# Kernel optimization log

Measured on AMD Instinct MI355X. Metric: run time of the kernel, lower is better.

## Reference

```python
import jax, jax.numpy as jnp
import numpy as np

HEADS = 4
DIM_HEAD = 32
DIM = 128
HIDDEN = HEADS * DIM_HEAD  # 128
SCALE = DIM_HEAD ** -0.5


def setup_inputs() -> dict:
    key = jax.random.key(0)
    ks = jax.random.split(key, 7)
    b, c, h, w = 4, DIM, 256, 256
    x = jax.random.normal(ks[0], (b, c, h, w), dtype=jnp.float32)
    context = jax.random.normal(ks[1], (b, c, h, w), dtype=jnp.float32)
    # conv1x1 weights stored as [out, in] matrices
    s_in = 1.0 / np.sqrt(DIM)
    Wq = jax.random.uniform(ks[2], (HIDDEN, DIM), jnp.float32, -s_in, s_in)
    Wk = jax.random.uniform(ks[3], (HIDDEN, DIM), jnp.float32, -s_in, s_in)
    Wv = jax.random.uniform(ks[4], (HIDDEN, DIM), jnp.float32, -s_in, s_in)
    s_h = 1.0 / np.sqrt(HIDDEN)
    Wo = jax.random.uniform(ks[5], (DIM, HIDDEN), jnp.float32, -s_h, s_h)
    bo = jax.random.uniform(ks[6], (DIM,), jnp.float32, -s_h, s_h)
    return {"x": x, "context": context, "Wq": Wq, "Wk": Wk, "Wv": Wv, "Wo": Wo, "bo": bo}


def reference(x, context, Wq, Wk, Wv, Wo, bo):
    b, c, h, w = x.shape
    n = h * w
    xf = x.reshape(b, c, n)         # flatten spatial
    cf = context.reshape(b, c, n)
    # conv1x1 projections == channel matmuls
    q = jnp.einsum('oc,bcn->bon', Wq, xf).reshape(b, HEADS, DIM_HEAD, n)
    k = jnp.einsum('oc,bcn->bon', Wk, cf).reshape(b, HEADS, DIM_HEAD, n)
    v = jnp.einsum('oc,bcn->bon', Wv, cf).reshape(b, HEADS, DIM_HEAD, n)
    q = q * SCALE
    k = jax.nn.softmax(k, axis=-1)  # softmax over spatial positions
    ctx = jnp.einsum('bhdn,bhen->bhde', k, v)   # [b,h,d,e] small d_head x d_head
    out = jnp.einsum('bhde,bhdn->bhen', ctx, q)  # [b,h,e,n]
    out = out.reshape(b, HIDDEN, n)
    out = jnp.einsum('oc,bcn->bon', Wo, out) + bo[None, :, None]
    return out.reshape(b, c, h, w)
```

## Files before the change

kernel.cpp:

```cpp
#include <hip/hip_runtime.h>
#include <cstdint>
#include <cstddef>

typedef __bf16 bf16x8 __attribute__((ext_vector_type(8)));
typedef float f32x4 __attribute__((ext_vector_type(4)));
typedef float f32x16 __attribute__((ext_vector_type(16)));
typedef unsigned int u32x2 __attribute__((ext_vector_type(2)));
typedef unsigned int u32x4 __attribute__((ext_vector_type(4)));

#define MFMA16(a, b, c) __builtin_amdgcn_mfma_f32_16x16x32_bf16((a), (b), (c), 0, 0, 0)
#define MFMA32(a, b, c) __builtin_amdgcn_mfma_f32_32x32x16_bf16((a), (b), (c), 0, 0, 0)

#define BAR() asm volatile("s_waitcnt lgkmcnt(0)\n\ts_barrier" ::: "memory")

static constexpr int CD = 128;
static constexpr int NTOK = 65536;
static constexpr float F_SCALE = 0.17677669529663688f;
static constexpr float F_LOG2E = 1.4426950408889634f;
static constexpr int PART = 4224;
static constexpr int NPARTS = 128;

__device__ __forceinline__ unsigned pk2(float a, float b) {
  unsigned short ua = __builtin_bit_cast(unsigned short, (__bf16)a);
  unsigned short ub = __builtin_bit_cast(unsigned short, (__bf16)b);
  return (unsigned)ua | ((unsigned)ub << 16);
}

__device__ __forceinline__ f32x16 z16() {
  f32x16 v;
#pragma unroll
  for (int i = 0; i < 16; ++i) v[i] = 0.f;
  return v;
}

struct Grp { f32x4 M[4]; };

__device__ __forceinline__ Grp load_grp(const float* src, int lane) {
  Grp g;
  const float* p = src + (size_t)((lane >> 4) * 4) * NTOK + (lane & 15) * 4;
#pragma unroll
  for (int v = 0; v < 4; ++v) g.M[v] = *(const f32x4*)(p + (size_t)v * NTOK);
  return g;
}

__device__ __forceinline__ void pack_grp(const Grp& g, char* T2, int cqBase, int lane) {
  int cq = cqBase + (lane >> 4);
  int nq = lane & 15;
#pragma unroll
  for (int j = 0; j < 4; ++j) {
    int n = nq * 4 + j;
    *(u32x2*)(T2 + n * 256 + ((cq * 8) ^ ((((n & 15) ^ (n >> 4))) << 4))) =
        u32x2{pk2(g.M[0][j], g.M[1][j]), pk2(g.M[2][j], g.M[3][j])};
  }
}

struct Grp32 { f32x4 M[4]; };

__device__ __forceinline__ Grp32 load_grp32(const float* src, int lane) {
  Grp32 g;
  int q = (lane >> 3) & 7;
  const float* p = src + (size_t)(2 * q) * NTOK + (lane & 7) * 4;
  g.M[0] = *(const f32x4*)p;
  g.M[1] = *(const f32x4*)(p + NTOK);
  g.M[2] = *(const f32x4*)(p + (size_t)16 * NTOK);
  g.M[3] = *(const f32x4*)(p + (size_t)17 * NTOK);
  return g;
}

__device__ __forceinline__ void pack_grp32(const Grp32& g, char* T2, int cpBase, int lane) {
  int q = (lane >> 3) & 7;
  int a = lane & 7;
#pragma unroll
  for (int j = 0; j < 4; ++j) {
    int n = a * 4 + j;
    int sw = (((n & 15) ^ (n >> 4)) << 4);
    *(unsigned*)(T2 + n * 256 + (((cpBase + q) * 4) ^ sw)) = pk2(g.M[0][j], g.M[1][j]);
    *(unsigned*)(T2 + n * 256 + (((cpBase + 8 + q) * 4) ^ sw)) = pk2(g.M[2][j], g.M[3][j]);
  }
}

__global__ __launch_bounds__(256) __attribute__((amdgpu_waves_per_eu(2)))
void k1_ctx(const float* __restrict__ ctx_in, const float* __restrict__ Wk,
            const float* __restrict__ Wv, float* __restrict__ S_part) {
  __shared__ char smem[32 * 1024];
  const int tid = threadIdx.x;
  const int lane = tid & 63;
  const int w = tid >> 6;
  const int l31 = lane & 31;
  const int l2 = lane >> 5;
  const int b = blockIdx.x >> 7;
  const int cb = blockIdx.x & 127;

  bf16x8 WfK[8], WfV[8];
#pragma unroll
  for (int ks = 0; ks < 8; ++ks) {
    const float* pK = Wk + (size_t)(w * 32 + l31) * CD + ks * 16 + l2 * 8;
    const float* pV = Wv + (size_t)(w * 32 + l31) * CD + ks * 16 + l2 * 8;
#pragma unroll
    for (int e = 0; e < 8; ++e) {
      WfK[ks][e] = (__bf16)(pK[e] * F_LOG2E);
      WfV[ks][e] = (__bf16)pV[e];
    }
  }

  f32x16 Sacc = z16();
  float zacc = 0.f;

  const float* srcA = ctx_in + (size_t)b * CD * NTOK + (size_t)(w * 32) * NTOK + cb * 512;
  const float* srcB = srcA + (size_t)16 * NTOK;

  Grp fa = load_grp(srcA, lane), fb = load_grp(srcB, lane);
#pragma unroll
  for (int s = 0; s < 8; ++s) {
    char* T2 = smem + (s & 1) * 16384;
    pack_grp(fa, T2, w * 8, lane);
    pack_grp(fb, T2, w * 8 + 4, lane);
    if (s < 7) {
      fa = load_grp(srcA + (s + 1) * 64, lane);
      fb = load_grp(srcB + (s + 1) * 64, lane);
    }
    BAR();

    unsigned pe[2][4][2], pv[2][4][2];
#pragma unroll
    for (int t = 0; t < 2; ++t) {
      f32x16 aK = z16(), aV = z16();
#pragma unroll
      for (int ks = 0; ks < 8; ++ks) {
        bf16x8 At = *(const bf16x8*)(
            T2 + (t * 32 + l31) * 256 +
            ((ks * 32 + l2 * 16) ^ (((l31 & 15) ^ (2 * t + (l31 >> 4))) << 4)));
        aK = MFMA32(At, WfK[ks], aK);
        aV = MFMA32(At, WfV[ks], aV);
      }
#pragma unroll
      for (int q = 0; q < 4; ++q) {
        float e0 = __builtin_exp2f(aK[4 * q + 0]);
        float e1 = __builtin_exp2f(aK[4 * q + 1]);
        float e2 = __builtin_exp2f(aK[4 * q + 2]);
        float e3 = __builtin_exp2f(aK[4 * q + 3]);
        zacc += (e0 + e1) + (e2 + e3);
        pe[t][q][0] = pk2(e0, e1);
        pe[t][q][1] = pk2(e2, e3);
        pv[t][q][0] = pk2(aV[4 * q + 0], aV[4 * q + 1]);
        pv[t][q][1] = pk2(aV[4 * q + 2], aV[4 * q + 3]);
      }
    }

#pragma unroll
    for (int nw = 0; nw < 4; ++nw) {
      const int t = nw >> 1, w2 = nw & 1;
      unsigned ea0 = pe[t][2 * w2][0], eb0 = pe[t][2 * w2 + 1][0];
      unsigned ea1 = pe[t][2 * w2][1], eb1 = pe[t][2 * w2 + 1][1];
      asm("v_permlane32_swap_b32 %0, %1" : "+v"(ea0), "+v"(eb0));
      asm("v_permlane32_swap_b32 %0, %1" : "+v"(ea1), "+v"(eb1));
      unsigned va0 = pv[t][2 * w2][0], vb0 = pv[t][2 * w2 + 1][0];
      unsigned va1 = pv[t][2 * w2][1], vb1 = pv[t][2 * w2 + 1][1];
      asm("v_permlane32_swap_b32 %0, %1" : "+v"(va0), "+v"(vb0));
      asm("v_permlane32_swap_b32 %0, %1" : "+v"(va1), "+v"(vb1));
      bf16x8 Ea = __builtin_bit_cast(bf16x8, u32x4{ea0, ea1, eb0, eb1});
      bf16x8 Vb = __builtin_bit_cast(bf16x8, u32x4{va0, va1, vb0, vb1});
      Sacc = MFMA32(Ea, Vb, Sacc);
    }
  }

  float* outp = S_part + (size_t)blockIdx.x * PART;
#pragma unroll
  for (int q = 0; q < 4; ++q) {
    f32x4 v{Sacc[4 * q + 0], Sacc[4 * q + 1], Sacc[4 * q + 2], Sacc[4 * q + 3]};
    *(f32x4*)(outp + w * 1024 + lane * 16 + q * 4) = v;
  }
  zacc += __shfl_xor(zacc, 32, 64);
  if (l2 == 0) outp[4096 + w * 32 + l31] = zacc;
}

__global__ void k2a_reduce(const float* __restrict__ S_part, float* __restrict__ S_red,
                           float* __restrict__ Z_red) {
  int bid = blockIdx.x;
  int b = bid / 33, bs = bid % 33;
  int tid = threadIdx.x;
  __shared__ float red[256];
  int e_loc = tid & 127, half = tid >> 7;
  const float* base =
      S_part + (size_t)b * NPARTS * PART + (bs < 32 ? bs * 128 + e_loc : 4096 + e_loc);
  float sum = 0.f;
  int h = NPARTS >> 1;
  for (int p = half * h; p < half * h + h; ++p) sum += base[(size_t)p * PART];
  red[tid] = sum;
  __syncthreads();
  if (tid < 128) {
    float v = red[tid] + red[tid + 128];
    if (bs < 32)
      S_red[b * 4096 + bs * 128 + tid] = v;
    else
      Z_red[b * 128 + tid] = v;
  }
}

__global__ void k2b_weff(const float* __restrict__ S_red, const float* __restrict__ Z_red,
                         const float* __restrict__ Wq, const float* __restrict__ Wo,
                         float* __restrict__ W_eff) {
  int b = blockIdx.x >> 3, og = blockIdx.x & 7;
  int tid = threadIdx.x;
  __shared__ float ctx_lds[4096];
  __shared__ float T_lds[16 * 128];
  for (int i = tid * 16; i < tid * 16 + 16; ++i) {
    int h = i >> 10, d = (i >> 5) & 31, e = i & 31;
    int fl = h * 1024 + ((e + ((d >> 2) & 1) * 32) << 4) + (d & 3) + ((d >> 3) << 2);
    ctx_lds[i] = S_red[b * 4096 + fl] / Z_red[b * 128 + h * 32 + d];
  }
  __syncthreads();
  {
    int o_loc = tid >> 4, hd0 = (tid & 15) * 8;
    int o = og * 16 + o_loc;
    for (int j = 0; j < 8; ++j) {
      int hd = hd0 + j, h = hd >> 5, d = hd & 31;
      const float* wo = Wo + o * 128 + h * 32;
      const float* cx = ctx_lds + h * 1024 + d * 32;
      float acc = 0.f;
      for (int e = 0; e < 32; ++e) acc += wo[e] * cx[e];
      T_lds[o_loc * 128 + hd] = acc;
    }
  }
  __syncthreads();
  {
    int o_loc = tid >> 4, c0 = (tid & 15) * 8;
    float acc[8] = {};
    const float* Trow = T_lds + o_loc * 128;
    for (int hd = 0; hd < 128; ++hd) {
      float tv = Trow[hd];
      const float* wq = Wq + hd * 128 + c0;
#pragma unroll
      for (int j = 0; j < 8; ++j) acc[j] += tv * wq[j];
    }
    float* op = W_eff + b * 16384 + (og * 16 + o_loc) * 128 + c0;
#pragma unroll
    for (int j = 0; j < 8; ++j) op[j] = F_SCALE * acc[j];
  }
}

__global__ __launch_bounds__(256, 2) void k3_out(const float* __restrict__ x,
                                                 const float* __restrict__ W_eff,
                                                 const float* __restrict__ bo,
                                                 float* __restrict__ out) {
  __shared__ char smem[16 * 1024];
  const int tid = threadIdx.x;
  const int lane = tid & 63;
  const int w = tid >> 6;
  const int l15 = lane & 15;
  const int lg = lane >> 4;
  const int b = blockIdx.x >> 8;
  const int cb = blockIdx.x & 255;

  bf16x8 Wf[2][4];
#pragma unroll
  for (int m = 0; m < 2; ++m) {
    int o = w * 32 + m * 16 + l15;
#pragma unroll
    for (int ks = 0; ks < 4; ++ks) {
      const float* p = W_eff + b * 16384 + o * 128 + ks * 32 + lg * 8;
#pragma unroll
      for (int e = 0; e < 8; ++e) Wf[m][ks][e] = (__bf16)p[e];
    }
  }
  float bof[2] = {bo[w * 32 + l15], bo[w * 32 + 16 + l15]};

  const float* src = x + (size_t)b * CD * NTOK + (size_t)(w * 32) * NTOK + cb * 256;
  float* dst = out + (size_t)b * CD * NTOK + cb * 256;

  Grp32 f0 = load_grp32(src, lane);
  Grp32 f1 = load_grp32(src + 32, lane);
  Grp32 f2 = load_grp32(src + 64, lane);

  f32x4 acc[8][2][2];
#pragma unroll
  for (int s = 0; s < 8; ++s)
#pragma unroll
    for (int t = 0; t < 2; ++t)
#pragma unroll
      for (int m = 0; m < 2; ++m) acc[s][t][m] = f32x4{0.f, 0.f, 0.f, 0.f};

#pragma unroll
  for (int s = 0; s < 8; ++s) {
    char* T2 = smem + (s & 1) * 8192;
    if ((s % 3) == 0) {
      pack_grp32(f0, T2, w * 16, lane);
      if (s + 3 < 8) f0 = load_grp32(src + (s + 3) * 32, lane);
    } else if ((s % 3) == 1) {
      pack_grp32(f1, T2, w * 16, lane);
      if (s + 3 < 8) f1 = load_grp32(src + (s + 3) * 32, lane);
    } else {
      pack_grp32(f2, T2, w * 16, lane);
      if (s + 3 < 8) f2 = load_grp32(src + (s + 3) * 32, lane);
    }
    BAR();

#pragma unroll
    for (int t = 0; t < 2; ++t) {
#pragma unroll
      for (int ks = 0; ks < 4; ++ks) {
        bf16x8 At = *(const bf16x8*)(T2 + (t * 16 + l15) * 256 +
                                     ((ks * 64 + lg * 16) ^ ((l15 ^ t) << 4)));
#pragma unroll
        for (int m = 0; m < 2; ++m) acc[s][t][m] = MFMA16(At, Wf[m][ks], acc[s][t][m]);
      }
    }
  }

#pragma unroll
  for (int m = 0; m < 2; ++m) {
    int o = w * 32 + m * 16 + l15;
    float bb = bof[m];
    float* rowp = dst + (size_t)o * NTOK;
#pragma unroll
    for (int s = 0; s < 8; ++s)
#pragma unroll
      for (int t = 0; t < 2; ++t) {
        f32x4 v = acc[s][t][m];
        v[0] += bb; v[1] += bb; v[2] += bb; v[3] += bb;
        *(f32x4*)(rowp + s * 32 + t * 16 + lg * 4) = v;
      }
  }
}

extern "C" void kernel_launch(void* const* d_in, const int* in_sizes, int n_in,
                              void* d_out, int out_size, void* d_ws, size_t ws_size,
                              hipStream_t stream) {
  const float* x = (const float*)d_in[0];
  const float* ctxg = (const float*)d_in[1];
  const float* Wq = (const float*)d_in[2];
  const float* Wk = (const float*)d_in[3];
  const float* Wv = (const float*)d_in[4];
  const float* Wo = (const float*)d_in[5];
  const float* bo = (const float*)d_in[6];
  float* out = (float*)d_out;

  float* ws = (float*)d_ws;
  float* S_part = ws;
  float* S_red = ws + (size_t)512 * PART;
  float* Z_red = S_red + 16384;
  float* W_eff = Z_red + 512;

  k1_ctx<<<dim3(512), dim3(256), 0, stream>>>(ctxg, Wk, Wv, S_part);
  k2a_reduce<<<dim3(132), dim3(256), 0, stream>>>(S_part, S_red, Z_red);
  k2b_weff<<<dim3(32), dim3(256), 0, stream>>>(S_red, Z_red, Wq, Wo, W_eff);
  k3_out<<<dim3(1024), dim3(256), 0, stream>>>(x, W_eff, bo, out);
}
```

Before: 154.7 us.

## Shrink k1 strips to 32 tokens, halve LDS, raise occupancy and grid size

The context-projection kernel now processes 32-token strips instead of 64, using a 16KB double buffer and the existing 32-row load/pack helpers, with a launch bound targeting 3 blocks per CU. When the workspace is large enough the grid grows to 1024 blocks of 8 strips each, otherwise 512 blocks of 16 strips, and the reduce kernel takes the part count as a parameter. The aim is more resident waves and more blocks to hide global-load latency. The cost is more per-strip barriers, twice as many partial sums to reduce, and a dynamic loop that is no longer unrolled.

```diff
diff --git a/kernel.cpp b/kernel.cpp
--- a/kernel.cpp
+++ b/kernel.cpp
@@ -18,7 +18,6 @@
 static constexpr float F_SCALE = 0.17677669529663688f;
 static constexpr float F_LOG2E = 1.4426950408889634f;
 static constexpr int PART = 4224;
-static constexpr int NPARTS = 128;
 
 __device__ __forceinline__ unsigned pk2(float a, float b) {
   unsigned short ua = __builtin_bit_cast(unsigned short, (__bf16)a);
@@ -31,27 +30,6 @@
 #pragma unroll
   for (int i = 0; i < 16; ++i) v[i] = 0.f;
   return v;
-}
-
-struct Grp { f32x4 M[4]; };
-
-__device__ __forceinline__ Grp load_grp(const float* src, int lane) {
-  Grp g;
-  const float* p = src + (size_t)((lane >> 4) * 4) * NTOK + (lane & 15) * 4;
-#pragma unroll
-  for (int v = 0; v < 4; ++v) g.M[v] = *(const f32x4*)(p + (size_t)v * NTOK);
-  return g;
-}
-
-__device__ __forceinline__ void pack_grp(const Grp& g, char* T2, int cqBase, int lane) {
-  int cq = cqBase + (lane >> 4);
-  int nq = lane & 15;
-#pragma unroll
-  for (int j = 0; j < 4; ++j) {
-    int n = nq * 4 + j;
-    *(u32x2*)(T2 + n * 256 + ((cq * 8) ^ ((((n & 15) ^ (n >> 4))) << 4))) =
-        u32x2{pk2(g.M[0][j], g.M[1][j]), pk2(g.M[2][j], g.M[3][j])};
-  }
 }
 
 struct Grp32 { f32x4 M[4]; };
@@ -79,17 +57,18 @@
   }
 }
 
-__global__ __launch_bounds__(256) __attribute__((amdgpu_waves_per_eu(2)))
-void k1_ctx(const float* __restrict__ ctx_in, const float* __restrict__ Wk,
-            const float* __restrict__ Wv, float* __restrict__ S_part) {
-  __shared__ char smem[32 * 1024];
+__global__ __launch_bounds__(256, 3) void k1_ctx(
+    const float* __restrict__ ctx_in, const float* __restrict__ Wk,
+    const float* __restrict__ Wv, float* __restrict__ S_part,
+    int cpb_log2, int nstrips) {
+  __shared__ char smem[16 * 1024];
   const int tid = threadIdx.x;
   const int lane = tid & 63;
   const int w = tid >> 6;
   const int l31 = lane & 31;
   const int l2 = lane >> 5;
-  const int b = blockIdx.x >> 7;
-  const int cb = blockIdx.x & 127;
+  const int b = blockIdx.x >> cpb_log2;
+  const int cb = blockIdx.x & ((1 << cpb_log2) - 1);
 
   bf16x8 WfK[8], WfV[8];
 #pragma unroll
@@ -106,56 +85,47 @@
   f32x16 Sacc = z16();
   float zacc = 0.f;
 
-  const float* srcA = ctx_in + (size_t)b * CD * NTOK + (size_t)(w * 32) * NTOK + cb * 512;
-  const float* srcB = srcA + (size_t)16 * NTOK;
-
-  Grp fa = load_grp(srcA, lane), fb = load_grp(srcB, lane);
-#pragma unroll
-  for (int s = 0; s < 8; ++s) {
-    char* T2 = smem + (s & 1) * 16384;
-    pack_grp(fa, T2, w * 8, lane);
-    pack_grp(fb, T2, w * 8 + 4, lane);
-    if (s < 7) {
-      fa = load_grp(srcA + (s + 1) * 64, lane);
-      fb = load_grp(srcB + (s + 1) * 64, lane);
-    }
+  const float* srcW =
+      ctx_in + (size_t)b * CD * NTOK + (size_t)(w * 32) * NTOK + cb * (nstrips * 32);
+  const int rdsw = ((l31 & 15) ^ (l31 >> 4)) << 4;
+
+  Grp32 f = load_grp32(srcW, lane);
+  for (int s = 0; s < nstrips; ++s) {
+    char* T2 = smem + (s & 1) * 8192;
+    pack_grp32(f, T2, w * 16, lane);
+    if (s + 1 < nstrips) f = load_grp32(srcW + (s + 1) * 32, lane);
     BAR();
 
-    unsigned pe[2][4][2], pv[2][4][2];
-#pragma unroll
-    for (int t = 0; t < 2; ++t) {
-      f32x16 aK = z16(), aV = z16();
-#pragma unroll
-      for (int ks = 0; ks < 8; ++ks) {
-        bf16x8 At = *(const bf16x8*)(
-            T2 + (t * 32 + l31) * 256 +
-            ((ks * 32 + l2 * 16) ^ (((l31 & 15) ^ (2 * t + (l31 >> 4))) << 4)));
-        aK = MFMA32(At, WfK[ks], aK);
-        aV = MFMA32(At, WfV[ks], aV);
-      }
-#pragma unroll
-      for (int q = 0; q < 4; ++q) {
-        float e0 = __builtin_exp2f(aK[4 * q + 0]);
-        float e1 = __builtin_exp2f(aK[4 * q + 1]);
-        float e2 = __builtin_exp2f(aK[4 * q + 2]);
-        float e3 = __builtin_exp2f(aK[4 * q + 3]);
-        zacc += (e0 + e1) + (e2 + e3);
-        pe[t][q][0] = pk2(e0, e1);
-        pe[t][q][1] = pk2(e2, e3);
-        pv[t][q][0] = pk2(aV[4 * q + 0], aV[4 * q + 1]);
-        pv[t][q][1] = pk2(aV[4 * q + 2], aV[4 * q + 3]);
-      }
-    }
-
-#pragma unroll
-    for (int nw = 0; nw < 4; ++nw) {
-      const int t = nw >> 1, w2 = nw & 1;
-      unsigned ea0 = pe[t][2 * w2][0], eb0 = pe[t][2 * w2 + 1][0];
-      unsigned ea1 = pe[t][2 * w2][1], eb1 = pe[t][2 * w2 + 1][1];
+    f32x16 aK = z16(), aV = z16();
+#pragma unroll
+    for (int ks = 0; ks < 8; ++ks) {
+      bf16x8 At = *(const bf16x8*)(T2 + l31 * 256 + ((ks * 32 + l2 * 16) ^ rdsw));
+      aK = MFMA32(At, WfK[ks], aK);
+      aV = MFMA32(At, WfV[ks], aV);
+    }
+
+    unsigned pe[4][2], pv[4][2];
+#pragma unroll
+    for (int q = 0; q < 4; ++q) {
+      float e0 = __builtin_exp2f(aK[4 * q + 0]);
+      float e1 = __builtin_exp2f(aK[4 * q + 1]);
+      float e2 = __builtin_exp2f(aK[4 * q + 2]);
+      float e3 = __builtin_exp2f(aK[4 * q + 3]);
+      zacc += (e0 + e1) + (e2 + e3);
+      pe[q][0] = pk2(e0, e1);
+      pe[q][1] = pk2(e2, e3);
+      pv[q][0] = pk2(aV[4 * q + 0], aV[4 * q + 1]);
+      pv[q][1] = pk2(aV[4 * q + 2], aV[4 * q + 3]);
+    }
+
+#pragma unroll
+    for (int w2 = 0; w2 < 2; ++w2) {
+      unsigned ea0 = pe[2 * w2][0], eb0 = pe[2 * w2 + 1][0];
+      unsigned ea1 = pe[2 * w2][1], eb1 = pe[2 * w2 + 1][1];
       asm("v_permlane32_swap_b32 %0, %1" : "+v"(ea0), "+v"(eb0));
       asm("v_permlane32_swap_b32 %0, %1" : "+v"(ea1), "+v"(eb1));
-      unsigned va0 = pv[t][2 * w2][0], vb0 = pv[t][2 * w2 + 1][0];
-      unsigned va1 = pv[t][2 * w2][1], vb1 = pv[t][2 * w2 + 1][1];
+      unsigned va0 = pv[2 * w2][0], vb0 = pv[2 * w2 + 1][0];
+      unsigned va1 = pv[2 * w2][1], vb1 = pv[2 * w2 + 1][1];
       asm("v_permlane32_swap_b32 %0, %1" : "+v"(va0), "+v"(vb0));
       asm("v_permlane32_swap_b32 %0, %1" : "+v"(va1), "+v"(vb1));
       bf16x8 Ea = __builtin_bit_cast(bf16x8, u32x4{ea0, ea1, eb0, eb1});
@@ -175,16 +145,16 @@
 }
 
 __global__ void k2a_reduce(const float* __restrict__ S_part, float* __restrict__ S_red,
-                           float* __restrict__ Z_red) {
+                           float* __restrict__ Z_red, int nparts) {
   int bid = blockIdx.x;
   int b = bid / 33, bs = bid % 33;
   int tid = threadIdx.x;
   __shared__ float red[256];
   int e_loc = tid & 127, half = tid >> 7;
   const float* base =
-      S_part + (size_t)b * NPARTS * PART + (bs < 32 ? bs * 128 + e_loc : 4096 + e_loc);
+      S_part + (size_t)b * nparts * PART + (bs < 32 ? bs * 128 + e_loc : 4096 + e_loc);
   float sum = 0.f;
-  int h = NPARTS >> 1;
+  int h = nparts >> 1;
   for (int p = half * h; p < half * h + h; ++p) sum += base[(size_t)p * PART];
   red[tid] = sum;
   __syncthreads();
@@ -335,14 +305,21 @@
   const float* bo = (const float*)d_in[6];
   float* out = (float*)d_out;
 
+  size_t need1024 = ((size_t)1024 * PART + 16384 + 512 + 65536) * sizeof(float);
+  int cpb_log2, nstrips;
+  if (ws_size >= need1024) { cpb_log2 = 8; nstrips = 8; }
+  else                     { cpb_log2 = 7; nstrips = 16; }
+  int nblk1 = 4 << cpb_log2;
+  int nparts = 1 << cpb_log2;
+
   float* ws = (float*)d_ws;
   float* S_part = ws;
-  float* S_red = ws + (size_t)512 * PART;
+  float* S_red = ws + (size_t)nblk1 * PART;
   float* Z_red = S_red + 16384;
   float* W_eff = Z_red + 512;
 
-  k1_ctx<<<dim3(512), dim3(256), 0, stream>>>(ctxg, Wk, Wv, S_part);
-  k2a_reduce<<<dim3(132), dim3(256), 0, stream>>>(S_part, S_red, Z_red);
+  k1_ctx<<<dim3(nblk1), dim3(256), 0, stream>>>(ctxg, Wk, Wv, S_part, cpb_log2, nstrips);
+  k2a_reduce<<<dim3(132), dim3(256), 0, stream>>>(S_part, S_red, Z_red, nparts);
   k2b_weff<<<dim3(32), dim3(256), 0, stream>>>(S_red, Z_red, Wq, Wo, W_eff);
   k3_out<<<dim3(1024), dim3(256), 0, stream>>>(x, W_eff, bo, out);
 }
```

New measurement: 173.9 us. 12.4% more time.
